# Kernel tuning notes

Measured on AMD Instinct MI355X. Metric: run time of the kernel, lower is better.

The kernel has to match this reference:

```python
import jax, jax.numpy as jnp
import numpy as np

def setup_inputs() -> dict:
    key = jax.random.key(0)
    k1, k2 = jax.random.split(key)
    B, T = 256, 100000
    x = jax.random.normal(k1, (B, T), dtype=jnp.float32)
    shifts = jax.random.randint(k2, (B,), 0, 1000, dtype=jnp.int32)
    return {"x": x, "shifts": shifts}

def reference(x, shifts):
    # tf.roll(x[i], shift=s, axis=0): out[j] = x[(j - s) % T]
    B, T = x.shape
    idx = (jnp.arange(T, dtype=jnp.int32)[None, :] - shifts[:, None]) % T  # [B, T]
    return jnp.take_along_axis(x, idx, axis=1)
```

## Files before the change

### kernel.cpp

```cpp
#include <hip/hip_runtime.h>

__global__ void roll_rows_realign(const float* __restrict__ x,
                                  const int* __restrict__ shifts,
                                  float* __restrict__ out,
                                  int T, int T4) {
    const int b = blockIdx.y;
    const int v = blockIdx.x * blockDim.x + threadIdx.x;
    if (v >= T4) return;

    int s = shifts[b] % T;
    if (s < 0) s += T;

    const int j = v * 4;
    int i = j - s;
    if (i < 0) i += T;

    const int a = i & 3;
    const int i4 = i - a;
    int i4b = i4 + 4;
    if (i4b >= T) i4b -= T;

    const float* __restrict__ xr = x + (size_t)b * (size_t)T;
    const float4 A = *reinterpret_cast<const float4*>(xr + i4);

    float4 r;
    if (a == 0) {
        r = A;
    } else {
        const float4 Bv = *reinterpret_cast<const float4*>(xr + i4b);
        switch (a) {
            case 1: r.x = A.y;  r.y = A.z;  r.z = A.w;  r.w = Bv.x; break;
            case 2: r.x = A.z;  r.y = A.w;  r.z = Bv.x; r.w = Bv.y; break;
            default: r.x = A.w; r.y = Bv.x; r.z = Bv.y; r.w = Bv.z; break;
        }
    }

    *reinterpret_cast<float4*>(out + (size_t)b * (size_t)T + j) = r;
}

__global__ void roll_rows_scalar(const float* __restrict__ x,
                                 const int* __restrict__ shifts,
                                 float* __restrict__ out,
                                 int T) {
    const int b = blockIdx.y;
    const int j = blockIdx.x * blockDim.x + threadIdx.x;
    if (j >= T) return;
    int s = shifts[b] % T;
    if (s < 0) s += T;
    int i = j - s;
    if (i < 0) i += T;
    out[(size_t)b * T + j] = x[(size_t)b * T + i];
}

extern "C" void kernel_launch(void* const* d_in, const int* in_sizes, int n_in,
                              void* d_out, int out_size, void* d_ws, size_t ws_size,
                              hipStream_t stream) {
    const float* x = (const float*)d_in[0];
    const int* shifts = (const int*)d_in[1];
    float* out = (float*)d_out;

    const int B = in_sizes[1];
    const int T = in_sizes[0] / B;

    if ((T & 3) == 0) {
        const int T4 = T / 4;
        dim3 block(256);
        dim3 grid((T4 + 255) / 256, B);
        roll_rows_realign<<<grid, block, 0, stream>>>(x, shifts, out, T, T4);
    } else {
        dim3 block(256);
        dim3 grid((T + 255) / 256, B);
        roll_rows_scalar<<<grid, block, 0, stream>>>(x, shifts, out, T);
    }
}
```

Baseline: 175.0 us.

## Use persistent chunked blocks per row with block-uniform templated realignment

Replaces the one-float4-per-thread grid with a fixed grid of 8 blocks per row. Each block loops over a contiguous chunk of the row with unrolled grid-stride iterations. The shift alignment is computed once per block and dispatched to a template specialization, which removes per-thread branching on alignment and the recomputation of shift math. This lowers block launch overhead and increases memory-level parallelism per thread, but the grid shrinks to 2048 blocks, which may limit occupancy on a GPU with many CUs.

```diff
diff --git a/kernel.cpp b/kernel.cpp
--- a/kernel.cpp
+++ b/kernel.cpp
@@ -1,41 +1,82 @@
 #include <hip/hip_runtime.h>
 
-__global__ void roll_rows_realign(const float* __restrict__ x,
-                                  const int* __restrict__ shifts,
-                                  float* __restrict__ out,
-                                  int T, int T4) {
+#define BLOCK 256
+#define CHUNKS 8
+
+
+template <int ASEL>
+__device__ __forceinline__ void roll_chunk(const float* __restrict__ xr,
+                                           float* __restrict__ outr,
+                                           int T, int sa, int v0, int vend) {
+    const int nfull = (vend - v0) / BLOCK;
+    int v = v0 + (int)threadIdx.x;
+
+#pragma unroll 4
+    for (int k = 0; k < nfull; ++k, v += BLOCK) {
+        const int j = v << 2;
+        int i4 = j - sa;
+        if (i4 < 0) i4 += T;
+        const float4 A = *reinterpret_cast<const float4*>(xr + i4);
+        float4 r;
+        if constexpr (ASEL == 0) {
+            r = A;
+        } else {
+            int i4b = i4 + 4;
+            if (i4b >= T) i4b -= T;
+            const float4 Bv = *reinterpret_cast<const float4*>(xr + i4b);
+            if constexpr (ASEL == 1)      r = make_float4(A.y, A.z, A.w, Bv.x);
+            else if constexpr (ASEL == 2) r = make_float4(A.z, A.w, Bv.x, Bv.y);
+            else                          r = make_float4(A.w, Bv.x, Bv.y, Bv.z);
+        }
+        *reinterpret_cast<float4*>(outr + j) = r;
+    }
+
+    if (v < vend) {
+        const int j = v << 2;
+        int i4 = j - sa;
+        if (i4 < 0) i4 += T;
+        const float4 A = *reinterpret_cast<const float4*>(xr + i4);
+        float4 r;
+        if constexpr (ASEL == 0) {
+            r = A;
+        } else {
+            int i4b = i4 + 4;
+            if (i4b >= T) i4b -= T;
+            const float4 Bv = *reinterpret_cast<const float4*>(xr + i4b);
+            if constexpr (ASEL == 1)      r = make_float4(A.y, A.z, A.w, Bv.x);
+            else if constexpr (ASEL == 2) r = make_float4(A.z, A.w, Bv.x, Bv.y);
+            else                          r = make_float4(A.w, Bv.x, Bv.y, Bv.z);
+        }
+        *reinterpret_cast<float4*>(outr + j) = r;
+    }
+}
+
+__global__ __launch_bounds__(BLOCK)
+void roll_rows_chunked(const float* __restrict__ x,
+                       const int* __restrict__ shifts,
+                       float* __restrict__ out,
+                       int T, int T4) {
     const int b = blockIdx.y;
-    const int v = blockIdx.x * blockDim.x + threadIdx.x;
-    if (v >= T4) return;
+    const float* __restrict__ xr = x + (size_t)b * (size_t)T;
+    float* __restrict__ outr = out + (size_t)b * (size_t)T;
 
     int s = shifts[b] % T;
     if (s < 0) s += T;
+    const int a = (-s) & 3;
+    int sa = s + a;
+    if (sa >= T) sa -= T;
 
-    const int j = v * 4;
-    int i = j - s;
-    if (i < 0) i += T;
+    const int cnt = (T4 + CHUNKS - 1) / CHUNKS;
+    const int v0 = blockIdx.x * cnt;
+    const int vend = min(v0 + cnt, T4);
+    if (v0 >= vend) return;
 
-    const int a = i & 3;
-    const int i4 = i - a;
-    int i4b = i4 + 4;
-    if (i4b >= T) i4b -= T;
-
-    const float* __restrict__ xr = x + (size_t)b * (size_t)T;
-    const float4 A = *reinterpret_cast<const float4*>(xr + i4);
-
-    float4 r;
-    if (a == 0) {
-        r = A;
-    } else {
-        const float4 Bv = *reinterpret_cast<const float4*>(xr + i4b);
-        switch (a) {
-            case 1: r.x = A.y;  r.y = A.z;  r.z = A.w;  r.w = Bv.x; break;
-            case 2: r.x = A.z;  r.y = A.w;  r.z = Bv.x; r.w = Bv.y; break;
-            default: r.x = A.w; r.y = Bv.x; r.z = Bv.y; r.w = Bv.z; break;
-        }
+    switch (a) {
+        case 0:  roll_chunk<0>(xr, outr, T, sa, v0, vend); break;
+        case 1:  roll_chunk<1>(xr, outr, T, sa, v0, vend); break;
+        case 2:  roll_chunk<2>(xr, outr, T, sa, v0, vend); break;
+        default: roll_chunk<3>(xr, outr, T, sa, v0, vend); break;
     }
-
-    *reinterpret_cast<float4*>(out + (size_t)b * (size_t)T + j) = r;
 }
 
 __global__ void roll_rows_scalar(const float* __restrict__ x,
@@ -64,9 +105,9 @@
 
     if ((T & 3) == 0) {
         const int T4 = T / 4;
-        dim3 block(256);
-        dim3 grid((T4 + 255) / 256, B);
-        roll_rows_realign<<<grid, block, 0, stream>>>(x, shifts, out, T, T4);
+        dim3 block(BLOCK);
+        dim3 grid(CHUNKS, B);
+        roll_rows_chunked<<<grid, block, 0, stream>>>(x, shifts, out, T, T4);
     } else {
         dim3 block(256);
         dim3 grid((T + 255) / 256, B);
```

Measured after the change: 194.2 us. 11.0% more time.

## Hoist per-row alignment switch, use nontemporal stores, two vectors per thread

Applied to the files above, without the earlier changes.

Computes the misalignment from the row shift once per block and dispatches to a templated path, so the per-element branch on alignment disappears. Each thread now handles two float4 outputs, which halves the grid, and writes them with nontemporal stores to avoid polluting the cache with output data. This trades some occupancy for more memory-level parallelism per thread. The wrap-around handling is kept per vector.

```diff
diff --git a/kernel.cpp b/kernel.cpp
--- a/kernel.cpp
+++ b/kernel.cpp
@@ -1,41 +1,71 @@
 #include <hip/hip_runtime.h>
 
-__global__ void roll_rows_realign(const float* __restrict__ x,
-                                  const int* __restrict__ shifts,
-                                  float* __restrict__ out,
-                                  int T, int T4) {
+#define BLOCK 256
+#define VPT 2
+
+typedef float f32x4 __attribute__((ext_vector_type(4)));
+
+
+template <int ASEL>
+__device__ __forceinline__ f32x4 fetch4(const float* __restrict__ xr, int T, int i4) {
+    const f32x4 A = *reinterpret_cast<const f32x4*>(xr + i4);
+    if constexpr (ASEL == 0) {
+        return A;
+    } else {
+        int i4b = i4 + 4;
+        if (i4b >= T) i4b -= T;
+        const f32x4 Bv = *reinterpret_cast<const f32x4*>(xr + i4b);
+        f32x4 r;
+        if constexpr (ASEL == 1)      { r.x = A.y; r.y = A.z; r.z = A.w; r.w = Bv.x; }
+        else if constexpr (ASEL == 2) { r.x = A.z; r.y = A.w; r.z = Bv.x; r.w = Bv.y; }
+        else                          { r.x = A.w; r.y = Bv.x; r.z = Bv.y; r.w = Bv.z; }
+        return r;
+    }
+}
+
+template <int ASEL>
+__device__ __forceinline__ void do_pair(const float* __restrict__ xr,
+                                        float* __restrict__ outr,
+                                        int T, int T4, int sa,
+                                        int v1, int v2) {
+    if (v1 < T4) {
+        const int j1 = v1 << 2;
+        int i1 = j1 - sa; if (i1 < 0) i1 += T;
+        const f32x4 r1 = fetch4<ASEL>(xr, T, i1);
+        if (v2 < T4) {
+            const int j2 = v2 << 2;
+            int i2 = j2 - sa; if (i2 < 0) i2 += T;
+            const f32x4 r2 = fetch4<ASEL>(xr, T, i2);
+            __builtin_nontemporal_store(r2, reinterpret_cast<f32x4*>(outr + j2));
+        }
+        __builtin_nontemporal_store(r1, reinterpret_cast<f32x4*>(outr + j1));
+    }
+}
+
+__global__ __launch_bounds__(BLOCK)
+void roll_rows_nt(const float* __restrict__ x,
+                  const int* __restrict__ shifts,
+                  float* __restrict__ out,
+                  int T, int T4) {
     const int b = blockIdx.y;
-    const int v = blockIdx.x * blockDim.x + threadIdx.x;
-    if (v >= T4) return;
+    const float* __restrict__ xr = x + (size_t)b * (size_t)T;
+    float* __restrict__ outr = out + (size_t)b * (size_t)T;
 
     int s = shifts[b] % T;
     if (s < 0) s += T;
+    const int a = (-s) & 3;
+    int sa = s + a;
+    if (sa >= T) sa -= T;
 
-    const int j = v * 4;
-    int i = j - s;
-    if (i < 0) i += T;
+    const int v1 = blockIdx.x * (BLOCK * VPT) + (int)threadIdx.x;
+    const int v2 = v1 + BLOCK;
 
-    const int a = i & 3;
-    const int i4 = i - a;
-    int i4b = i4 + 4;
-    if (i4b >= T) i4b -= T;
-
-    const float* __restrict__ xr = x + (size_t)b * (size_t)T;
-    const float4 A = *reinterpret_cast<const float4*>(xr + i4);
-
-    float4 r;
-    if (a == 0) {
-        r = A;
-    } else {
-        const float4 Bv = *reinterpret_cast<const float4*>(xr + i4b);
-        switch (a) {
-            case 1: r.x = A.y;  r.y = A.z;  r.z = A.w;  r.w = Bv.x; break;
-            case 2: r.x = A.z;  r.y = A.w;  r.z = Bv.x; r.w = Bv.y; break;
-            default: r.x = A.w; r.y = Bv.x; r.z = Bv.y; r.w = Bv.z; break;
-        }
+    switch (a) {
+        case 0:  do_pair<0>(xr, outr, T, T4, sa, v1, v2); break;
+        case 1:  do_pair<1>(xr, outr, T, T4, sa, v1, v2); break;
+        case 2:  do_pair<2>(xr, outr, T, T4, sa, v1, v2); break;
+        default: do_pair<3>(xr, outr, T, T4, sa, v1, v2); break;
     }
-
-    *reinterpret_cast<float4*>(out + (size_t)b * (size_t)T + j) = r;
 }
 
 __global__ void roll_rows_scalar(const float* __restrict__ x,
@@ -64,9 +94,9 @@
 
     if ((T & 3) == 0) {
         const int T4 = T / 4;
-        dim3 block(256);
-        dim3 grid((T4 + 255) / 256, B);
-        roll_rows_realign<<<grid, block, 0, stream>>>(x, shifts, out, T, T4);
+        dim3 block(BLOCK);
+        dim3 grid((T4 + BLOCK * VPT - 1) / (BLOCK * VPT), B);
+        roll_rows_nt<<<grid, block, 0, stream>>>(x, shifts, out, T, T4);
     } else {
         dim3 block(256);
         dim3 grid((T + 255) / 256, B);
```

Result: no change. 177.6 us (+1.5%).
